# Kernel optimization log

Hardware: AMD Instinct MI355X
Metric: run time of the kernel (lower is better)

Reference implementation:

```python
import jax, jax.numpy as jnp
import numpy as np

LN_EPS = 1e-3  # keras LayerNormalization default epsilon


def setup_inputs() -> dict:
    key = jax.random.key(0)
    ks = jax.random.split(key, 6)
    B, H, W, C = 8, 64, 64, 256
    s = 1.0 / np.sqrt(C)
    return {
        "x": jax.random.normal(ks[0], (B, H, W, C), jnp.float32),
        "gamma": jnp.ones((C,), jnp.float32),
        "beta": jnp.zeros((C,), jnp.float32),
        "wq": jax.random.normal(ks[1], (C, C), jnp.float32) * s,
        "bq": jnp.zeros((C,), jnp.float32),
        "wk": jax.random.normal(ks[2], (C, C), jnp.float32) * s,
        "bk": jnp.zeros((C,), jnp.float32),
        "wv": jax.random.normal(ks[3], (C, C), jnp.float32) * s,
        "bv": jnp.zeros((C,), jnp.float32),
        "wo": jax.random.normal(ks[4], (C, C), jnp.float32) * s,
        "bo": jnp.zeros((C,), jnp.float32),
    }


def reference(x, gamma, beta, wq, bq, wk, bk, wv, bv, wo, bo):
    B, H, W, C = x.shape
    # LayerNormalization over channel axis (keras default axis=-1, eps=1e-3)
    mean = jnp.mean(x, axis=-1, keepdims=True)
    var = jnp.mean(jnp.square(x - mean), axis=-1, keepdims=True)
    h = (x - mean) * jax.lax.rsqrt(var + LN_EPS) * gamma + beta

    q = h @ wq + bq
    k = h @ wk + bk
    v = h @ wv + bv

    # flatten spatial dims: single-head attention over N = H*W positions
    N = H * W
    qf = q.reshape(B, N, C)
    kf = k.reshape(B, N, C)
    vf = v.reshape(B, N, C)

    scale = jnp.asarray(C, x.dtype) ** -0.5
    scores = jnp.einsum('bnc,bmc->bnm', qf, kf) * scale  # [B, N, N]
    attn = jax.nn.softmax(scores, axis=-1)
    o = jnp.einsum('bnm,bmc->bnc', attn, vf).reshape(B, H, W, C)

    o = o @ wo + bo
    return x + o
```

## Files before the change

kernel.cpp:

```cpp
#include <hip/hip_runtime.h>
#include <hip/hip_bf16.h>
#include <stdint.h>

typedef __attribute__((ext_vector_type(8))) short bf16x8;
typedef __attribute__((ext_vector_type(4))) short s16x4;
typedef __attribute__((ext_vector_type(4))) float f32x4;

__device__ __forceinline__ unsigned short f2b(float x) {
  __hip_bfloat16 h = __float2bfloat16(x);
  unsigned short u;
  __builtin_memcpy(&u, &h, 2);
  return u;
}

__device__ __forceinline__ float b2f(unsigned short u) {
  unsigned v = (unsigned)u << 16;
  float f;
  __builtin_memcpy(&f, &v, 4);
  return f;
}

__device__ __forceinline__ void glds16(const void* g, void* l) {
  __builtin_amdgcn_global_load_lds((const __attribute__((address_space(1))) void*)g,
                                   (__attribute__((address_space(3))) void*)l,
                                   16, 0, 0);
}

#define LQ_LDS (80 * 1024)

__global__ __launch_bounds__(256, 2) void ln_qkv(
    const float* __restrict__ x, const float* __restrict__ gamma,
    const float* __restrict__ beta, const unsigned short* __restrict__ wT,
    const float* __restrict__ bq, const float* __restrict__ bk,
    const float* __restrict__ bv,
    unsigned short* __restrict__ q, unsigned short* __restrict__ kk,
    unsigned short* __restrict__ vT, float qscale)
{
  extern __shared__ char lds[];
  const int t = threadIdx.x;
  const int lane = t & 63;
  const int w = t >> 6;
  const int wr = w >> 1, wc = w & 1;
  const long long row0 = (long long)blockIdx.y * 128;
  const int col0 = blockIdx.x * 128;

  const int sr = t >> 2;
  const int sc = (t & 3) * 8;

  auto stageB = [&](int st, int c) {
    const unsigned short* gb = wT + (st >> 3) * 65536 +
                               (long long)(col0 + sr) * 256 + (st & 7) * 32 + sc;
    char* d = lds + 65536 + c * 8192 + w * 1024;
    glds16(gb, d);
    glds16(gb + 64 * 256, d + 4096);
  };

  stageB(0, 0);

  {
    const f32x4 g4 = *(const f32x4*)(gamma + lane * 4);
    const f32x4 b4 = *(const f32x4*)(beta + lane * 4);
    for (int rr = 0; rr < 32; rr++) {
      const int rl = w * 32 + rr;
      const f32x4 v = *(const f32x4*)(x + (row0 + rl) * 256 + lane * 4);
      float s = v[0] + v[1] + v[2] + v[3];
      float s2 = v[0] * v[0] + v[1] * v[1] + v[2] * v[2] + v[3] * v[3];
#pragma unroll
      for (int o = 32; o >= 1; o >>= 1) {
        s += __shfl_xor(s, o, 64);
        s2 += __shfl_xor(s2, o, 64);
      }
      const float mean = s * (1.f / 256.f);
      const float var = s2 * (1.f / 256.f) - mean * mean;
      const float rstd = rsqrtf(var + 1e-3f);
      s16x4 hv;
#pragma unroll
      for (int e = 0; e < 4; e++) hv[e] = (short)f2b((v[e] - mean) * rstd * g4[e] + b4[e]);
      *(s16x4*)(lds + ((rl * 512 + lane * 8) ^ ((rl & 7) << 4))) = hv;
    }
  }

  const int l15 = lane & 15;
  const int l4 = lane >> 4;
  int step = 0;
#pragma unroll
  for (int z = 0; z < 3; z++) {
    f32x4 acc[4][4] = {};
#pragma unroll
    for (int k0 = 0; k0 < 8; k0++, step++) {
      const int cur = step & 1;
      __syncthreads();
      if (step < 23) stageB(step + 1, cur ^ 1);
      bf16x8 a[4], b[4];
#pragma unroll
      for (int i = 0; i < 4; i++) {
        const int row = wr * 64 + i * 16 + l15;
        a[i] = *(const bf16x8*)(lds + ((row * 512 + k0 * 64 + l4 * 16) ^ ((l15 & 7) << 4)));
      }
      const char* pb = lds + 65536 + cur * 8192;
#pragma unroll
      for (int j = 0; j < 4; j++)
        b[j] = *(const bf16x8*)(pb + (wc * 64 + j * 16 + l15) * 64 + l4 * 16);
#pragma unroll
      for (int i = 0; i < 4; i++)
#pragma unroll
        for (int j = 0; j < 4; j++)
          acc[i][j] = __builtin_amdgcn_mfma_f32_16x16x32_bf16(a[i], b[j], acc[i][j], 0, 0, 0);
    }
    const float* bias = z == 0 ? bq : z == 1 ? bk : bv;
    const float scale = z == 0 ? qscale : 1.0f;
#pragma unroll
    for (int i = 0; i < 4; i++) {
#pragma unroll
      for (int j = 0; j < 4; j++) {
        const int col = col0 + wc * 64 + j * 16 + l15;
        const float bv_ = bias[col];
#pragma unroll
        for (int r = 0; r < 4; r++) {
          const long long row = row0 + wr * 64 + i * 16 + l4 * 4 + r;
          const float val = (acc[i][j][r] + bv_) * scale;
          if (z == 0) {
            q[row * 256 + col] = f2b(val);
          } else if (z == 1) {
            kk[row * 256 + col] = f2b(val);
          } else {
            const int bb = (int)(row >> 12), rr = (int)(row & 4095);
            const int kl = rr & 31;
            const int rrp = (rr & ~31) |
                            ((((kl >> 2) & 3) << 3) | (((kl >> 4) & 1) << 2) | (kl & 3));
            vT[((long long)bb * 256 + col) * 4096 + rrp] = f2b(val);
          }
        }
      }
    }
  }
}

__global__ __launch_bounds__(256) void gemm_out(
    const unsigned short* __restrict__ o0, const unsigned short* __restrict__ o1,
    const float2* __restrict__ ml0, const float2* __restrict__ ml1,
    const unsigned short* __restrict__ Bt,
    float* __restrict__ C, const float* __restrict__ bias,
    const float* __restrict__ resid)
{
  __shared__ unsigned short As[128 * 32];
  __shared__ unsigned short Bs[128 * 32];
  const int t = threadIdx.x;
  const int lane = t & 63;
  const int wv_ = t >> 6;
  const int wr = wv_ >> 1, wc = wv_ & 1;
  const long long row0 = (long long)blockIdx.y * 128;
  const int col0 = blockIdx.x * 128;

  const int sr = t >> 2;
  const int sc = (t & 3) * 8;
  const long long ar0 = row0 + sr;
  float f0a, f1a, f0b, f1b;
  {
    const float2 a = ml0[ar0], c = ml1[ar0];
    const float M = fmaxf(a.x, c.x);
    const float w0 = exp2f(a.x - M), w1 = exp2f(c.x - M);
    const float inv = 1.f / (w0 * a.y + w1 * c.y);
    f0a = w0 * inv;
    f1a = w1 * inv;
  }
  {
    const float2 a = ml0[ar0 + 64], c = ml1[ar0 + 64];
    const float M = fmaxf(a.x, c.x);
    const float w0 = exp2f(a.x - M), w1 = exp2f(c.x - M);
    const float inv = 1.f / (w0 * a.y + w1 * c.y);
    f0b = w0 * inv;
    f1b = w1 * inv;
  }
  const unsigned short* g0 = o0 + ar0 * 256 + sc;
  const unsigned short* g1 = o1 + ar0 * 256 + sc;
  const unsigned short* gb = Bt + (col0 + sr) * 256 + sc;
  char* lB = (char*)Bs + (t >> 6) * 1024;

  const int l15 = lane & 15;
  const int l4 = lane >> 4;
  const unsigned short* pa = As + (wr * 64 + l15) * 32 + l4 * 8;
  const unsigned short* pb = Bs + (wc * 64 + l15) * 32 + l4 * 8;

  f32x4 acc[4][4] = {};

  for (int k0 = 0; k0 < 256; k0 += 32) {
    bf16x8 u0 = *(const bf16x8*)g0;
    bf16x8 u1 = *(const bf16x8*)g1;
    bf16x8 v0 = *(const bf16x8*)(g0 + 64 * 256);
    bf16x8 v1 = *(const bf16x8*)(g1 + 64 * 256);
    bf16x8 m0, m1;
#pragma unroll
    for (int e = 0; e < 8; e++) {
      m0[e] = (short)f2b(f0a * b2f((unsigned short)u0[e]) + f1a * b2f((unsigned short)u1[e]));
      m1[e] = (short)f2b(f0b * b2f((unsigned short)v0[e]) + f1b * b2f((unsigned short)v1[e]));
    }
    *(bf16x8*)((char*)As + t * 16) = m0;
    *(bf16x8*)((char*)As + 4096 + t * 16) = m1;
    glds16(gb, lB);
    glds16(gb + 64 * 256, lB + 4096);
    g0 += 32;
    g1 += 32;
    gb += 32;
    __syncthreads();
    bf16x8 a[4], b[4];
#pragma unroll
    for (int i = 0; i < 4; i++) a[i] = *(const bf16x8*)(pa + i * 512);
#pragma unroll
    for (int j = 0; j < 4; j++) b[j] = *(const bf16x8*)(pb + j * 512);
#pragma unroll
    for (int i = 0; i < 4; i++)
#pragma unroll
      for (int j = 0; j < 4; j++)
        acc[i][j] = __builtin_amdgcn_mfma_f32_16x16x32_bf16(a[i], b[j], acc[i][j], 0, 0, 0);
    __syncthreads();
  }

#pragma unroll
  for (int i = 0; i < 4; i++) {
#pragma unroll
    for (int j = 0; j < 4; j++) {
      const int col = col0 + wc * 64 + j * 16 + l15;
      const float bv_ = bias[col];
#pragma unroll
      for (int r = 0; r < 4; r++) {
        const long long row = row0 + wr * 64 + i * 16 + l4 * 4 + r;
        const long long idx = row * 256 + col;
        C[idx] = resid[idx] + acc[i][j][r] + bv_;
      }
    }
  }
}

__global__ void wtrans(const float* __restrict__ wq, const float* __restrict__ wk,
                       const float* __restrict__ wv, const float* __restrict__ wo,
                       unsigned short* __restrict__ wT)
{
  const float* w = blockIdx.z == 0 ? wq : blockIdx.z == 1 ? wk : blockIdx.z == 2 ? wv : wo;
  unsigned short* o = wT + (long long)blockIdx.z * 65536;
  __shared__ float tile[16][17];
  const int tx = threadIdx.x, ty = threadIdx.y;
  const int bx = blockIdx.x * 16, by = blockIdx.y * 16;
  tile[ty][tx] = w[(by + ty) * 256 + bx + tx];
  __syncthreads();
  o[(bx + ty) * 256 + (by + tx)] = f2b(tile[tx][ty]);
}

#define FL_LDS (64 * 1024)

__global__ __launch_bounds__(256, 2) void flash(
    const unsigned short* __restrict__ q,
    const unsigned short* __restrict__ kk,
    const unsigned short* __restrict__ vT,
    unsigned short* __restrict__ o0,
    unsigned short* __restrict__ o1,
    float2* __restrict__ ml0,
    float2* __restrict__ ml1)
{
  extern __shared__ char lds[];
  const int t = threadIdx.x;
  const int w = t >> 6;
  const int lane = t & 63;
  const int l15 = lane & 15, hi = lane >> 4;
  const int b = blockIdx.x & 7;
  const int kh = (blockIdx.x >> 3) & 1;
  const int qb = blockIdx.x >> 4;
  const long long qrow = (long long)b * 4096 + (long long)qb * 128 + w * 32;

  const unsigned short* kbase = kk + (long long)b * 4096 * 256 + (long long)kh * 2048 * 256;
  const unsigned short* vbase = vT + (long long)b * 256 * 4096 + kh * 2048;

  const int gs_k = (t & 31) ^ ((t >> 5) & 7);
  const unsigned short* Kst = kbase + (t >> 5) * 256 + gs_k * 8;
  const int gs_v = (t & 3) ^ ((t >> 2) & 3);
  const unsigned short* Vst = vbase + (long long)(t >> 2) * 4096 + gs_v * 8;

  bf16x8 Qf[2][8];
#pragma unroll
  for (int qg = 0; qg < 2; qg++) {
    const unsigned short* qp = q + (qrow + qg * 16 + l15) * 256 + hi * 8;
#pragma unroll
    for (int ks = 0; ks < 8; ks++) Qf[qg][ks] = *(const bf16x8*)(qp + ks * 32);
  }

  f32x4 O[2][16] = {};
  float mrow[2] = {-1e30f, -1e30f};
  float lrow[2] = {0.f, 0.f};

  auto stage = [&](int it, int c) {
    const unsigned short* ks_ = Kst + (long long)it * 32 * 256;
    const unsigned short* vs_ = Vst + it * 32;
    char* kd = lds + c * 16384 + w * 1024;
    char* vd = lds + 32768 + c * 16384 + w * 1024;
#pragma unroll
    for (int p = 0; p < 4; p++) {
      glds16(ks_ + p * 8 * 256, kd + p * 4096);
      glds16(vs_ + (long long)p * 64 * 4096, vd + p * 4096);
    }
  };

  stage(0, 0);

  for (int it = 0; it < 64; ++it) {
    const int cur = it & 1;
    __builtin_amdgcn_s_barrier();
    if (it < 63) {
      stage(it + 1, cur ^ 1);
      asm volatile("s_waitcnt vmcnt(8)" ::: "memory");
    } else {
      asm volatile("s_waitcnt vmcnt(0)" ::: "memory");
    }
    __builtin_amdgcn_sched_barrier(0);
    __builtin_amdgcn_s_barrier();
    const char* Kb = lds + cur * 16384;
    const char* Vb = lds + 32768 + cur * 16384;

    f32x4 S[2][2] = {};
    __builtin_amdgcn_s_setprio(1);
#pragma unroll
    for (int ks = 0; ks < 8; ks++) {
#pragma unroll
      for (int j = 0; j < 2; j++) {
        bf16x8 Kf = *(const bf16x8*)(Kb + (j * 16 + l15) * 512 +
                                     ((ks * 64 + hi * 16) ^ ((l15 & 7) << 4)));
        S[0][j] = __builtin_amdgcn_mfma_f32_16x16x32_bf16(Kf, Qf[0][ks], S[0][j], 0, 0, 0);
        S[1][j] = __builtin_amdgcn_mfma_f32_16x16x32_bf16(Kf, Qf[1][ks], S[1][j], 0, 0, 0);
      }
    }
    __builtin_amdgcn_s_setprio(0);

    bf16x8 Pf8[2];
#pragma unroll
    for (int qg = 0; qg < 2; qg++) {
      const float mxl =
          fmaxf(fmaxf(fmaxf(S[qg][0][0], S[qg][0][1]), fmaxf(S[qg][0][2], S[qg][0][3])),
                fmaxf(fmaxf(S[qg][1][0], S[qg][1][1]), fmaxf(S[qg][1][2], S[qg][1][3])));
      if (!__all(mxl <= mrow[qg] + 8.f)) {
        float mx = fmaxf(mxl, __shfl_xor(mxl, 16, 64));
        mx = fmaxf(mx, __shfl_xor(mx, 32, 64));
        const float mn = fmaxf(mrow[qg], mx);
        const float rs_ = exp2f(mrow[qg] - mn);
        mrow[qg] = mn;
        lrow[qg] *= rs_;
#pragma unroll
        for (int dg = 0; dg < 16; dg++) O[qg][dg] *= rs_;
      }
      float sum = 0.f;
      float e[2][4];
#pragma unroll
      for (int j = 0; j < 2; j++)
#pragma unroll
        for (int r = 0; r < 4; r++) {
          e[j][r] = exp2f(S[qg][j][r] - mrow[qg]);
          sum += e[j][r];
        }
      lrow[qg] += sum;
      bf16x8 p;
#pragma unroll
      for (int j = 0; j < 2; j++)
#pragma unroll
        for (int r = 0; r < 4; r++) p[j * 4 + r] = (short)f2b(e[j][r]);
      Pf8[qg] = p;
    }

    __builtin_amdgcn_s_setprio(1);
#pragma unroll
    for (int dg = 0; dg < 16; dg++) {
      bf16x8 Vf8 = *(const bf16x8*)(Vb + (dg * 16 + l15) * 64 +
                                    ((hi * 16) ^ ((l15 & 3) << 4)));
      O[0][dg] = __builtin_amdgcn_mfma_f32_16x16x32_bf16(Vf8, Pf8[0], O[0][dg], 0, 0, 0);
      O[1][dg] = __builtin_amdgcn_mfma_f32_16x16x32_bf16(Vf8, Pf8[1], O[1][dg], 0, 0, 0);
    }
    __builtin_amdgcn_s_setprio(0);
  }

  unsigned short* const op = kh ? o1 : o0;
  float2* const mlp = kh ? ml1 : ml0;
  __syncthreads();
  char* const slab = lds + w * 16384;
#pragma unroll
  for (int qg = 0; qg < 2; qg++) {
    float lr = lrow[qg];
    lr += __shfl_xor(lr, 16, 64);
    lr += __shfl_xor(lr, 32, 64);
#pragma unroll
    for (int dg = 0; dg < 16; dg++) {
      f32x4 v = O[qg][dg];
      *(f32x4*)(slab + l15 * 1024 + ((dg * 64 + hi * 16) ^ ((l15 & 7) << 4))) = v;
    }
    if (hi == 0) mlp[qrow + qg * 16 + l15] = make_float2(mrow[qg], lr);
    const int qq = lane >> 2;
    const int dc = lane & 3;
    const long long orow = (qrow + qg * 16 + qq) * 256 + dc * 64;
#pragma unroll
    for (int half = 0; half < 8; half++) {
      bf16x8 pack;
#pragma unroll
      for (int di = 0; di < 2; di++) {
        f32x4 v = *(const f32x4*)(slab + qq * 1024 +
                                  ((dc * 256 + half * 32 + di * 16) ^ ((qq & 7) << 4)));
#pragma unroll
        for (int e2 = 0; e2 < 4; e2++) pack[di * 4 + e2] = (short)f2b(v[e2]);
      }
      *(bf16x8*)(op + orow + half * 8) = pack;
    }
    __syncthreads();
  }
}

extern "C" void kernel_launch(void* const* d_in, const int* in_sizes, int n_in,
                              void* d_out, int out_size, void* d_ws, size_t ws_size,
                              hipStream_t stream)
{
  const float* x = (const float*)d_in[0];
  const float* gamma = (const float*)d_in[1];
  const float* beta = (const float*)d_in[2];
  const float* wq = (const float*)d_in[3];
  const float* bq = (const float*)d_in[4];
  const float* wk = (const float*)d_in[5];
  const float* bk = (const float*)d_in[6];
  const float* wv = (const float*)d_in[7];
  const float* bv = (const float*)d_in[8];
  const float* wo = (const float*)d_in[9];
  const float* bo = (const float*)d_in[10];

  const int Cc = 256;
  const long long MR = 32768;

  char* base = (char*)d_ws;
  size_t off = 0;
  auto take = [&](size_t bytes) -> char* {
    char* p = base + off;
    off = (off + bytes + 255) & ~(size_t)255;
    return p;
  };
  unsigned short* q   = (unsigned short*)take((size_t)MR * Cc * 2);
  unsigned short* kk  = (unsigned short*)take((size_t)MR * Cc * 2);
  unsigned short* vT  = (unsigned short*)take((size_t)MR * Cc * 2);
  unsigned short* o0  = (unsigned short*)take((size_t)MR * Cc * 2);
  unsigned short* o1  = (unsigned short*)take((size_t)MR * Cc * 2);
  unsigned short* wT  = (unsigned short*)take(4ull * Cc * Cc * 2);
  float2* ml0 = (float2*)take((size_t)MR * sizeof(float2));
  float2* ml1 = (float2*)take((size_t)MR * sizeof(float2));

  wtrans<<<dim3(16, 16, 4), dim3(16, 16), 0, stream>>>(wq, wk, wv, wo, wT);

  const float qscale = 0.0625f * 1.44269504f;
  ln_qkv<<<dim3(2, 256), dim3(256), LQ_LDS, stream>>>(x, gamma, beta, wT, bq, bk, bv,
                                                      q, kk, vT, qscale);

  flash<<<dim3(512), dim3(256), FL_LDS, stream>>>(q, kk, vT, o0, o1, ml0, ml1);

  gemm_out<<<dim3(2, 256, 1), 256, 0, stream>>>(o0, o1, ml0, ml1, wT + 3 * 65536,
                                                (float*)d_out, bo, x);
}
```

Measured before the change: 219.5 us.

## Split flash attention keys four ways with single-buffered LDS and merge in output GEMM

Raises the flash-attention split-K factor from two to four key chunks, doubling the grid to 1024 blocks, and drops LDS double buffering so each block uses 32 KB instead of 64 KB. The aim is more concurrent workgroups and better CU fill. The epilogue now converts to bf16 before the LDS staging pass, halving slab size. The cost is an explicit wait and barrier before every tile with no prefetch overlap, plus twice the partial-output traffic that gemm_out must read and merge.

Result: slower. 248.4 us (+13.2%).

```diff
diff --git a/kernel.cpp b/kernel.cpp
--- a/kernel.cpp
+++ b/kernel.cpp
@@ -138,7 +138,9 @@
 
 __global__ __launch_bounds__(256) void gemm_out(
     const unsigned short* __restrict__ o0, const unsigned short* __restrict__ o1,
+    const unsigned short* __restrict__ o2, const unsigned short* __restrict__ o3,
     const float2* __restrict__ ml0, const float2* __restrict__ ml1,
+    const float2* __restrict__ ml2, const float2* __restrict__ ml3,
     const unsigned short* __restrict__ Bt,
     float* __restrict__ C, const float* __restrict__ bias,
     const float* __restrict__ resid)
@@ -155,25 +157,24 @@
   const int sr = t >> 2;
   const int sc = (t & 3) * 8;
   const long long ar0 = row0 + sr;
-  float f0a, f1a, f0b, f1b;
-  {
-    const float2 a = ml0[ar0], c = ml1[ar0];
-    const float M = fmaxf(a.x, c.x);
+  float fA[2][4];
+#pragma unroll
+  for (int rr = 0; rr < 2; rr++) {
+    const long long row = ar0 + rr * 64;
+    const float2 a = ml0[row], c = ml1[row], d = ml2[row], e = ml3[row];
+    const float M = fmaxf(fmaxf(a.x, c.x), fmaxf(d.x, e.x));
     const float w0 = exp2f(a.x - M), w1 = exp2f(c.x - M);
-    const float inv = 1.f / (w0 * a.y + w1 * c.y);
-    f0a = w0 * inv;
-    f1a = w1 * inv;
-  }
-  {
-    const float2 a = ml0[ar0 + 64], c = ml1[ar0 + 64];
-    const float M = fmaxf(a.x, c.x);
-    const float w0 = exp2f(a.x - M), w1 = exp2f(c.x - M);
-    const float inv = 1.f / (w0 * a.y + w1 * c.y);
-    f0b = w0 * inv;
-    f1b = w1 * inv;
+    const float w2 = exp2f(d.x - M), w3 = exp2f(e.x - M);
+    const float inv = 1.f / (w0 * a.y + w1 * c.y + w2 * d.y + w3 * e.y);
+    fA[rr][0] = w0 * inv;
+    fA[rr][1] = w1 * inv;
+    fA[rr][2] = w2 * inv;
+    fA[rr][3] = w3 * inv;
   }
   const unsigned short* g0 = o0 + ar0 * 256 + sc;
   const unsigned short* g1 = o1 + ar0 * 256 + sc;
+  const unsigned short* g2 = o2 + ar0 * 256 + sc;
+  const unsigned short* g3 = o3 + ar0 * 256 + sc;
   const unsigned short* gb = Bt + (col0 + sr) * 256 + sc;
   char* lB = (char*)Bs + (t >> 6) * 1024;
 
@@ -185,22 +186,27 @@
   f32x4 acc[4][4] = {};
 
   for (int k0 = 0; k0 < 256; k0 += 32) {
-    bf16x8 u0 = *(const bf16x8*)g0;
-    bf16x8 u1 = *(const bf16x8*)g1;
-    bf16x8 v0 = *(const bf16x8*)(g0 + 64 * 256);
-    bf16x8 v1 = *(const bf16x8*)(g1 + 64 * 256);
-    bf16x8 m0, m1;
-#pragma unroll
-    for (int e = 0; e < 8; e++) {
-      m0[e] = (short)f2b(f0a * b2f((unsigned short)u0[e]) + f1a * b2f((unsigned short)u1[e]));
-      m1[e] = (short)f2b(f0b * b2f((unsigned short)v0[e]) + f1b * b2f((unsigned short)v1[e]));
-    }
-    *(bf16x8*)((char*)As + t * 16) = m0;
-    *(bf16x8*)((char*)As + 4096 + t * 16) = m1;
+#pragma unroll
+    for (int rr = 0; rr < 2; rr++) {
+      bf16x8 u0 = *(const bf16x8*)(g0 + rr * 64 * 256);
+      bf16x8 u1 = *(const bf16x8*)(g1 + rr * 64 * 256);
+      bf16x8 u2 = *(const bf16x8*)(g2 + rr * 64 * 256);
+      bf16x8 u3 = *(const bf16x8*)(g3 + rr * 64 * 256);
+      bf16x8 m_;
+#pragma unroll
+      for (int e = 0; e < 8; e++)
+        m_[e] = (short)f2b(fA[rr][0] * b2f((unsigned short)u0[e]) +
+                           fA[rr][1] * b2f((unsigned short)u1[e]) +
+                           fA[rr][2] * b2f((unsigned short)u2[e]) +
+                           fA[rr][3] * b2f((unsigned short)u3[e]));
+      *(bf16x8*)((char*)As + rr * 4096 + t * 16) = m_;
+    }
     glds16(gb, lB);
     glds16(gb + 64 * 256, lB + 4096);
     g0 += 32;
     g1 += 32;
+    g2 += 32;
+    g3 += 32;
     gb += 32;
     __syncthreads();
     bf16x8 a[4], b[4];
@@ -246,16 +252,16 @@
   o[(bx + ty) * 256 + (by + tx)] = f2b(tile[tx][ty]);
 }
 
-#define FL_LDS (64 * 1024)
+#define FL_LDS (32 * 1024)
 
 __global__ __launch_bounds__(256, 2) void flash(
     const unsigned short* __restrict__ q,
     const unsigned short* __restrict__ kk,
     const unsigned short* __restrict__ vT,
-    unsigned short* __restrict__ o0,
-    unsigned short* __restrict__ o1,
-    float2* __restrict__ ml0,
-    float2* __restrict__ ml1)
+    unsigned short* __restrict__ o0, unsigned short* __restrict__ o1,
+    unsigned short* __restrict__ o2, unsigned short* __restrict__ o3,
+    float2* __restrict__ ml0, float2* __restrict__ ml1,
+    float2* __restrict__ ml2, float2* __restrict__ ml3)
 {
   extern __shared__ char lds[];
   const int t = threadIdx.x;
@@ -263,12 +269,12 @@
   const int lane = t & 63;
   const int l15 = lane & 15, hi = lane >> 4;
   const int b = blockIdx.x & 7;
-  const int kh = (blockIdx.x >> 3) & 1;
-  const int qb = blockIdx.x >> 4;
+  const int kh = (blockIdx.x >> 3) & 3;
+  const int qb = blockIdx.x >> 5;
   const long long qrow = (long long)b * 4096 + (long long)qb * 128 + w * 32;
 
-  const unsigned short* kbase = kk + (long long)b * 4096 * 256 + (long long)kh * 2048 * 256;
-  const unsigned short* vbase = vT + (long long)b * 256 * 4096 + kh * 2048;
+  const unsigned short* kbase = kk + (long long)b * 4096 * 256 + (long long)kh * 1024 * 256;
+  const unsigned short* vbase = vT + (long long)b * 256 * 4096 + kh * 1024;
 
   const int gs_k = (t & 31) ^ ((t >> 5) & 7);
   const unsigned short* Kst = kbase + (t >> 5) * 256 + gs_k * 8;
@@ -287,11 +293,11 @@
   float mrow[2] = {-1e30f, -1e30f};
   float lrow[2] = {0.f, 0.f};
 
-  auto stage = [&](int it, int c) {
+  auto stage = [&](int it) {
     const unsigned short* ks_ = Kst + (long long)it * 32 * 256;
     const unsigned short* vs_ = Vst + it * 32;
-    char* kd = lds + c * 16384 + w * 1024;
-    char* vd = lds + 32768 + c * 16384 + w * 1024;
+    char* kd = lds + w * 1024;
+    char* vd = lds + 16384 + w * 1024;
 #pragma unroll
     for (int p = 0; p < 4; p++) {
       glds16(ks_ + p * 8 * 256, kd + p * 4096);
@@ -299,21 +305,14 @@
     }
   };
 
-  stage(0, 0);
-
-  for (int it = 0; it < 64; ++it) {
-    const int cur = it & 1;
-    __builtin_amdgcn_s_barrier();
-    if (it < 63) {
-      stage(it + 1, cur ^ 1);
-      asm volatile("s_waitcnt vmcnt(8)" ::: "memory");
-    } else {
-      asm volatile("s_waitcnt vmcnt(0)" ::: "memory");
-    }
+  stage(0);
+
+  for (int it = 0; it < 32; ++it) {
+    asm volatile("s_waitcnt vmcnt(0)" ::: "memory");
     __builtin_amdgcn_sched_barrier(0);
     __builtin_amdgcn_s_barrier();
-    const char* Kb = lds + cur * 16384;
-    const char* Vb = lds + 32768 + cur * 16384;
+    const char* Kb = lds;
+    const char* Vb = lds + 16384;
 
     f32x4 S[2][2] = {};
     __builtin_amdgcn_s_setprio(1);
@@ -372,12 +371,15 @@
       O[1][dg] = __builtin_amdgcn_mfma_f32_16x16x32_bf16(Vf8, Pf8[1], O[1][dg], 0, 0, 0);
     }
     __builtin_amdgcn_s_setprio(0);
-  }
-
-  unsigned short* const op = kh ? o1 : o0;
-  float2* const mlp = kh ? ml1 : ml0;
+
+    __builtin_amdgcn_s_barrier();
+    if (it < 31) stage(it + 1);
+  }
+
+  unsigned short* const op = kh == 0 ? o0 : kh == 1 ? o1 : kh == 2 ? o2 : o3;
+  float2* const mlp = kh == 0 ? ml0 : kh == 1 ? ml1 : kh == 2 ? ml2 : ml3;
   __syncthreads();
-  char* const slab = lds + w * 16384;
+  char* const slab = lds + w * 8192;
 #pragma unroll
   for (int qg = 0; qg < 2; qg++) {
     float lr = lrow[qg];
@@ -385,24 +387,20 @@
     lr += __shfl_xor(lr, 32, 64);
 #pragma unroll
     for (int dg = 0; dg < 16; dg++) {
-      f32x4 v = O[qg][dg];
-      *(f32x4*)(slab + l15 * 1024 + ((dg * 64 + hi * 16) ^ ((l15 & 7) << 4))) = v;
+      s16x4 pk;
+#pragma unroll
+      for (int r = 0; r < 4; r++) pk[r] = (short)f2b(O[qg][dg][r]);
+      *(s16x4*)(slab + l15 * 512 + ((dg * 32 + hi * 8) ^ ((l15 & 7) << 4))) = pk;
     }
     if (hi == 0) mlp[qrow + qg * 16 + l15] = make_float2(mrow[qg], lr);
     const int qq = lane >> 2;
     const int dc = lane & 3;
     const long long orow = (qrow + qg * 16 + qq) * 256 + dc * 64;
 #pragma unroll
-    for (int half = 0; half < 8; half++) {
-      bf16x8 pack;
-#pragma unroll
-      for (int di = 0; di < 2; di++) {
-        f32x4 v = *(const f32x4*)(slab + qq * 1024 +
-                                  ((dc * 256 + half * 32 + di * 16) ^ ((qq & 7) << 4)));
-#pragma unroll
-        for (int e2 = 0; e2 < 4; e2++) pack[di * 4 + e2] = (short)f2b(v[e2]);
-      }
-      *(bf16x8*)(op + orow + half * 8) = pack;
+    for (int st = 0; st < 8; st++) {
+      bf16x8 v = *(const bf16x8*)(slab + qq * 512 +
+                                  ((dc * 128 + st * 16) ^ ((qq & 7) << 4)));
+      *(bf16x8*)(op + orow + st * 8) = v;
     }
     __syncthreads();
   }
@@ -439,9 +437,13 @@
   unsigned short* vT  = (unsigned short*)take((size_t)MR * Cc * 2);
   unsigned short* o0  = (unsigned short*)take((size_t)MR * Cc * 2);
   unsigned short* o1  = (unsigned short*)take((size_t)MR * Cc * 2);
+  unsigned short* o2  = (unsigned short*)take((size_t)MR * Cc * 2);
+  unsigned short* o3  = (unsigned short*)take((size_t)MR * Cc * 2);
   unsigned short* wT  = (unsigned short*)take(4ull * Cc * Cc * 2);
   float2* ml0 = (float2*)take((size_t)MR * sizeof(float2));
   float2* ml1 = (float2*)take((size_t)MR * sizeof(float2));
+  float2* ml2 = (float2*)take((size_t)MR * sizeof(float2));
+  float2* ml3 = (float2*)take((size_t)MR * sizeof(float2));
 
   wtrans<<<dim3(16, 16, 4), dim3(16, 16), 0, stream>>>(wq, wk, wv, wo, wT);
 
@@ -449,8 +451,9 @@
   ln_qkv<<<dim3(2, 256), dim3(256), LQ_LDS, stream>>>(x, gamma, beta, wT, bq, bk, bv,
                                                       q, kk, vT, qscale);
 
-  flash<<<dim3(512), dim3(256), FL_LDS, stream>>>(q, kk, vT, o0, o1, ml0, ml1);
-
-  gemm_out<<<dim3(2, 256, 1), 256, 0, stream>>>(o0, o1, ml0, ml1, wT + 3 * 65536,
-                                                (float*)d_out, bo, x);
-}
+  flash<<<dim3(1024), dim3(256), FL_LDS, stream>>>(q, kk, vT, o0, o1, o2, o3,
+                                                   ml0, ml1, ml2, ml3);
+
+  gemm_out<<<dim3(2, 256, 1), 256, 0, stream>>>(o0, o1, o2, o3, ml0, ml1, ml2, ml3,
+                                                wT + 3 * 65536, (float*)d_out, bo, x);
+}
```
